# Kernel optimization log

Hardware: AMD Instinct MI355X
Metric: run time of the kernel (lower is better)

## Reference

```python
import jax, jax.numpy as jnp
import numpy as np

HIDDEN_DIM = 128


def setup_inputs() -> dict:
    key = jax.random.key(0)
    ks = jax.random.split(key, 7)
    n_edges, edge_dim, edge_hidden, d = 20000, 16, 128, HIDDEN_DIM
    h_v = jax.random.normal(ks[0], (n_edges, d), dtype=jnp.float32)
    h_w = jax.random.normal(ks[1], (n_edges, d), dtype=jnp.float32)
    edge_features = jax.random.normal(ks[2], (n_edges, edge_dim), dtype=jnp.float32)
    W1 = jax.random.normal(ks[3], (edge_dim, edge_hidden), dtype=jnp.float32) * (1.0 / np.sqrt(edge_dim))
    b1 = jnp.zeros((edge_hidden,), dtype=jnp.float32)
    W2 = jax.random.normal(ks[4], (edge_hidden, d * d), dtype=jnp.float32) * (1.0 / np.sqrt(edge_hidden))
    b2 = jnp.zeros((d * d,), dtype=jnp.float32)
    return {"h_v": h_v, "h_w": h_w, "edge_features": edge_features,
            "W1": W1, "b1": b1, "W2": W2, "b2": b2}


def reference(h_v, h_w, edge_features, W1, b1, W2, b2):
    d = HIDDEN_DIM
    # Edge MLP: edge_dim -> edge_hidden -> d*d
    hidden = jax.nn.relu(edge_features @ W1 + b1)          # (E, edge_hidden)
    A = (hidden @ W2 + b2).reshape(-1, d, d)               # (E, d, d) per-edge matrices
    # Batched matrix-vector product: messages_e = A_e @ h_w_e
    messages = jnp.einsum('eij,ej->ei', A, h_w)            # (E, d)
    return messages
```

## Files before the change

kernel.cpp:

```cpp
#include <hip/hip_runtime.h>

#define E_EDGES 20000
#define D_DIM   128
#define HS      136

#define NBA 136
#define NBH 313
#define NBC 320
#define NBD 250

#define SLAB_B 21504

typedef _Float16 f16x8 __attribute__((ext_vector_type(8)));
typedef _Float16 f16x2 __attribute__((ext_vector_type(2)));
typedef float    floatx4 __attribute__((ext_vector_type(4)));

union F8 { f16x8 v; f16x2 h2[4]; unsigned int u[4]; };

__device__ __forceinline__ unsigned short f32_to_f16(float f) {
    _Float16 h = (_Float16)f;
    return __builtin_bit_cast(unsigned short, h);
}

__device__ __forceinline__ void gload_lds16(const void* g, void* l) {
    __builtin_amdgcn_global_load_lds(
        (const __attribute__((address_space(1))) unsigned int*)g,
        (__attribute__((address_space(3))) unsigned int*)l, 16, 0, 0);
}

__global__ __launch_bounds__(256) void prep_all(
    const float* __restrict__ W2, const float* __restrict__ b2,
    const float* __restrict__ ef, const float* __restrict__ W1,
    const float* __restrict__ b1, const float* __restrict__ hw,
    uint4* __restrict__ bpf, char* __restrict__ hslab,
    unsigned short* __restrict__ hwb, float* __restrict__ outz)
{
    __shared__ __align__(16) char pmem[34816];
    const int bx = blockIdx.x;
    const int t  = threadIdx.x;

    if (bx < NBA) {
        const int h = bx;
        if (h < 129) {
            unsigned short* tile = (unsigned short*)pmem;
            const float* src = (h < 128) ? (W2 + (size_t)h * (D_DIM * D_DIM)) : b2;
            #pragma unroll
            for (int r = 0; r < 16; ++r) {
                const float4 v = ((const float4*)src)[r * 256 + t];
                int c   = (r * 256 + t) * 4;
                int col = c >> 7;
                int k   = c & 127;
                unsigned int u0 = f32_to_f16(v.x) | ((unsigned int)f32_to_f16(v.y) << 16);
                unsigned int u1 = f32_to_f16(v.z) | ((unsigned int)f32_to_f16(v.w) << 16);
                *(uint2*)&tile[col * 136 + k] = make_uint2(u0, u1);
            }
            __syncthreads();
            #pragma unroll
            for (int r2 = 0; r2 < 8; ++r2) {
                int cidx = r2 * 256 + t;
                int ll = cidx & 63;
                int nt = (cidx >> 6) & 3;
                int jq = (cidx >> 8) & 3;
                int ch = (cidx >> 10) & 1;
                int col = 64 * ch + 16 * nt + (ll & 15);
                int k0  = 32 * jq + 8 * (ll >> 4);
                bpf[(size_t)h * 2048 + cidx] = *(const uint4*)&tile[col * 136 + k0];
            }
        } else {
            #pragma unroll
            for (int r2 = 0; r2 < 8; ++r2)
                bpf[(size_t)h * 2048 + r2 * 256 + t] = make_uint4(0, 0, 0, 0);
        }
    } else if (bx < NBA + NBH) {
        float* W1s = (float*)pmem;
        float* b1s = (float*)(pmem + 8192);
        float (*efs)[17] = (float(*)[17])(pmem + 8704);
        const int b  = bx - NBA;
        const int e0 = b * 64;
        #pragma unroll
        for (int i = 0; i < 2; ++i)
            *(float4*)&W1s[(i * 256 + t) * 4] = ((const float4*)W1)[i * 256 + t];
        if (t < 32) *(float4*)&b1s[t * 4] = ((const float4*)b1)[t];
        {
            int e  = t >> 2;
            int k4 = (t & 3) * 4;
            int ge = e0 + e;
            float4 v = make_float4(0.f, 0.f, 0.f, 0.f);
            if (ge < E_EDGES) v = *(const float4*)(ef + (size_t)ge * 16 + k4);
            efs[e][k4 + 0] = v.x; efs[e][k4 + 1] = v.y;
            efs[e][k4 + 2] = v.z; efs[e][k4 + 3] = v.w;
        }
        __syncthreads();
        const int e  = t & 63;
        const int hg = t >> 6;
        const int ge = e0 + e;
        const bool valid = ge < E_EDGES;
        const int eg = ge / 80;
        const int re = ge - eg * 80;
        char* slab = hslab + (size_t)eg * SLAB_B + re * 264;
        float efr[16];
        #pragma unroll
        for (int k = 0; k < 16; ++k) efr[k] = efs[e][k];
        #pragma unroll 4
        for (int hi2 = 0; hi2 < 16; ++hi2) {
            const int h0 = hg * 32 + 2 * hi2;
            float2 bb = *(const float2*)&b1s[h0];
            float a0 = bb.x, a1 = bb.y;
            #pragma unroll
            for (int k = 0; k < 16; ++k) {
                float2 wv = *(const float2*)&W1s[k * 128 + h0];
                a0 += efr[k] * wv.x;
                a1 += efr[k] * wv.y;
            }
            unsigned int pk = (unsigned int)f32_to_f16(fmaxf(a0, 0.f))
                            | ((unsigned int)f32_to_f16(fmaxf(a1, 0.f)) << 16);
            if (valid) *(unsigned int*)(slab + h0 * 2) = pk;
        }
        if (hg == 0 && valid) {
            *(unsigned int*)(slab + 128 * 2) = 0x00003C00u;
            *(unsigned int*)(slab + 130 * 2) = 0u;
        }
    } else if (bx < NBA + NBH + NBC) {
        int i0 = (bx - NBA - NBH) * 256 + t;
        for (int i = i0; i < (E_EDGES * D_DIM) / 4; i += NBC * 256) {
            const float4 v = ((const float4*)hw)[i];
            union { unsigned short u16[4]; uint2 u2; } o;
            o.u16[0] = f32_to_f16(v.x);
            o.u16[1] = f32_to_f16(v.y);
            o.u16[2] = f32_to_f16(v.z);
            o.u16[3] = f32_to_f16(v.w);
            ((uint2*)hwb)[i] = o.u2;
        }
    } else {
        int i0 = (bx - NBA - NBH - NBC) * 256 + t;
        float4* o4 = (float4*)outz;
        for (int i = i0; i < (E_EDGES * D_DIM) / 4; i += NBD * 256)
            o4[i] = make_float4(0.f, 0.f, 0.f, 0.f);
    }
}

__global__ __launch_bounds__(256, 2)
void edge_main(const uint4* __restrict__ bpf, const char* __restrict__ hslab,
               const uint4* __restrict__ hwb, float* __restrict__ out) {
    __shared__ __align__(16) char slab[SLAB_B];
    const int bx  = blockIdx.x;
    const int ch  = (bx & 7) >> 2;
    const int eg  = (bx >> 3) * 4 + (bx & 3);
    if (eg >= 250) return;
    const int tid = threadIdx.x;
    const int jq  = tid >> 6;
    const int l   = tid & 63;
    const int l4  = l >> 4;
    const int lm  = l & 15;
    const int e0  = eg * 80;

    {
        const char* src = hslab + (size_t)eg * SLAB_B;
        for (int i = jq; i < 21; i += 4)
            gload_lds16(src + i * 1024 + l * 16, slab + i * 1024);
    }

    F8 hws[5];
    #pragma unroll
    for (int m = 0; m < 5; ++m)
        hws[m].v = ((const F8*)hwb)[(e0 + 16 * m + lm) * 16 + 4 * jq + l4].v;

    floatx4 C[5][4];
    #pragma unroll
    for (int m = 0; m < 5; ++m)
        #pragma unroll
        for (int nt = 0; nt < 4; ++nt)
            C[m][nt] = (floatx4){0.f, 0.f, 0.f, 0.f};

    __syncthreads();

    const f16x8* bpf8 = (const f16x8*)bpf;
    const int cbase = (ch * 4 + jq) * 256 + l;

    f16x8 B[2][4];
    auto loadB = [&](int h, f16x8 (&Bq)[4]) {
        const f16x8* p = bpf8 + (size_t)h * 2048 + cbase;
        #pragma unroll
        for (int nt = 0; nt < 4; ++nt)
            Bq[nt] = p[nt * 64];
    };
    auto loadHid = [&](int q, uint2 (&hid)[5]) {
        #pragma unroll
        for (int m = 0; m < 5; ++m)
            hid[m] = *(const uint2*)(slab + (16 * m + lm) * 264 + q * 8);
    };
    auto doH = [&](int h, const uint2 (&hid)[5]) {
        const int hh = h & 3, p = h & 1;
        #pragma unroll
        for (int m = 0; m < 5; ++m) {
            unsigned int s   = (hh < 2) ? hid[m].x : hid[m].y;
            unsigned int sel = (hh & 1) ? 0x03020302u : 0x01000100u;
            f16x2 d = __builtin_bit_cast(f16x2, __builtin_amdgcn_perm(0u, s, sel));
            F8 a;
            #pragma unroll
            for (int i = 0; i < 4; ++i) a.h2[i] = hws[m].h2[i] * d;
            #pragma unroll
            for (int nt = 0; nt < 4; ++nt)
                C[m][nt] = __builtin_amdgcn_mfma_f32_16x16x32_f16(a.v, B[p][nt], C[m][nt], 0, 0, 0);
        }
        loadB(h + 2, B[p]);
    };

    loadB(0, B[0]);
    loadB(1, B[1]);
    uint2 hidA[5], hidB[5];
    loadHid(0, hidA);
    for (int q = 0; q < 32; q += 2) {
        loadHid(q + 1, hidB);
        doH(4*q + 0, hidA); doH(4*q + 1, hidA); doH(4*q + 2, hidA); doH(4*q + 3, hidA);
        loadHid(q + 2, hidA);
        doH(4*q + 4, hidB); doH(4*q + 5, hidB); doH(4*q + 6, hidB); doH(4*q + 7, hidB);
    }
    doH(128, hidA); doH(129, hidA);
    doH(130, hidA); doH(131, hidA);

    #pragma unroll
    for (int m = 0; m < 5; ++m)
        #pragma unroll
        for (int nt = 0; nt < 4; ++nt)
            #pragma unroll
            for (int r = 0; r < 4; ++r)
                atomicAdd(&out[(size_t)(e0 + 16 * m + 4 * l4 + r) * D_DIM
                               + 64 * ch + 16 * nt + lm], C[m][nt][r]);
}

extern "C" void kernel_launch(void* const* d_in, const int* in_sizes, int n_in,
                              void* d_out, int out_size, void* d_ws, size_t ws_size,
                              hipStream_t stream) {
    const float* h_w = (const float*)d_in[1];
    const float* ef  = (const float*)d_in[2];
    const float* W1  = (const float*)d_in[3];
    const float* b1  = (const float*)d_in[4];
    const float* W2  = (const float*)d_in[5];
    const float* b2  = (const float*)d_in[6];
    float* out = (float*)d_out;

    char* ws = (char*)d_ws;
    uint4*          bpf   = (uint4*)ws;
    char*           hslab = ws + 4456448;
    unsigned short* hwb   = (unsigned short*)(ws + 4456448 + 5376000);

    hipLaunchKernelGGL(prep_all, dim3(NBA + NBH + NBC + NBD), dim3(256), 0, stream,
                       W2, b2, ef, W1, b1, h_w, bpf, hslab, hwb, out);
    hipLaunchKernelGGL(edge_main, dim3(504), dim3(256), 0, stream,
                       bpf, hslab, (const uint4*)hwb, out);
}
```

Baseline: 177.3 us.

## Split output columns four ways and reduce K-partials in LDS instead of atomics

Each block now covers 32 output columns instead of 64, with grid doubled to 1000 blocks and occupancy hint raised to 4 blocks per CU. The B-fragment layout in prep is reshuffled to match. The four waves' K-split partial sums are reduced through LDS, and wave 0 writes the result with plain stores. This removes the global float atomics and the separate zero-fill of the output. The trade-off is that each block re-reads the hidden slab and h_w, which roughly doubles L2 traffic for those, and the reduction adds several block barriers.

```diff
diff --git a/kernel.cpp b/kernel.cpp
--- a/kernel.cpp
+++ b/kernel.cpp
@@ -7,7 +7,6 @@
 #define NBA 136
 #define NBH 313
 #define NBC 320
-#define NBD 250
 
 #define SLAB_B 21504
 
@@ -33,7 +32,7 @@
     const float* __restrict__ ef, const float* __restrict__ W1,
     const float* __restrict__ b1, const float* __restrict__ hw,
     uint4* __restrict__ bpf, char* __restrict__ hslab,
-    unsigned short* __restrict__ hwb, float* __restrict__ outz)
+    unsigned short* __restrict__ hwb)
 {
     __shared__ __align__(16) char pmem[34816];
     const int bx = blockIdx.x;
@@ -59,10 +58,10 @@
             for (int r2 = 0; r2 < 8; ++r2) {
                 int cidx = r2 * 256 + t;
                 int ll = cidx & 63;
-                int nt = (cidx >> 6) & 3;
-                int jq = (cidx >> 8) & 3;
-                int ch = (cidx >> 10) & 1;
-                int col = 64 * ch + 16 * nt + (ll & 15);
+                int nt = (cidx >> 6) & 1;
+                int jq = (cidx >> 7) & 3;
+                int ch = (cidx >> 9) & 3;
+                int col = 32 * ch + 16 * nt + (ll & 15);
                 int k0  = 32 * jq + 8 * (ll >> 4);
                 bpf[(size_t)h * 2048 + cidx] = *(const uint4*)&tile[col * 136 + k0];
             }
@@ -120,7 +119,7 @@
             *(unsigned int*)(slab + 128 * 2) = 0x00003C00u;
             *(unsigned int*)(slab + 130 * 2) = 0u;
         }
-    } else if (bx < NBA + NBH + NBC) {
+    } else {
         int i0 = (bx - NBA - NBH) * 256 + t;
         for (int i = i0; i < (E_EDGES * D_DIM) / 4; i += NBC * 256) {
             const float4 v = ((const float4*)hw)[i];
@@ -131,22 +130,16 @@
             o.u16[3] = f32_to_f16(v.w);
             ((uint2*)hwb)[i] = o.u2;
         }
-    } else {
-        int i0 = (bx - NBA - NBH - NBC) * 256 + t;
-        float4* o4 = (float4*)outz;
-        for (int i = i0; i < (E_EDGES * D_DIM) / 4; i += NBD * 256)
-            o4[i] = make_float4(0.f, 0.f, 0.f, 0.f);
-    }
-}
-
-__global__ __launch_bounds__(256, 2)
+    }
+}
+
+__global__ __launch_bounds__(256, 4)
 void edge_main(const uint4* __restrict__ bpf, const char* __restrict__ hslab,
                const uint4* __restrict__ hwb, float* __restrict__ out) {
     __shared__ __align__(16) char slab[SLAB_B];
     const int bx  = blockIdx.x;
-    const int ch  = (bx & 7) >> 2;
-    const int eg  = (bx >> 3) * 4 + (bx & 3);
-    if (eg >= 250) return;
+    const int ch  = (bx & 7) >> 1;
+    const int eg  = (bx >> 3) * 2 + (bx & 1);
     const int tid = threadIdx.x;
     const int jq  = tid >> 6;
     const int l   = tid & 63;
@@ -165,29 +158,23 @@
     for (int m = 0; m < 5; ++m)
         hws[m].v = ((const F8*)hwb)[(e0 + 16 * m + lm) * 16 + 4 * jq + l4].v;
 
-    floatx4 C[5][4];
+    floatx4 C[5][2];
     #pragma unroll
     for (int m = 0; m < 5; ++m)
         #pragma unroll
-        for (int nt = 0; nt < 4; ++nt)
+        for (int nt = 0; nt < 2; ++nt)
             C[m][nt] = (floatx4){0.f, 0.f, 0.f, 0.f};
 
     __syncthreads();
 
     const f16x8* bpf8 = (const f16x8*)bpf;
-    const int cbase = (ch * 4 + jq) * 256 + l;
-
-    f16x8 B[2][4];
-    auto loadB = [&](int h, f16x8 (&Bq)[4]) {
+    const int cbase = ch * 512 + jq * 128 + l;
+
+    f16x8 B[2][2];
+    auto loadB = [&](int h, f16x8 (&Bq)[2]) {
         const f16x8* p = bpf8 + (size_t)h * 2048 + cbase;
-        #pragma unroll
-        for (int nt = 0; nt < 4; ++nt)
-            Bq[nt] = p[nt * 64];
-    };
-    auto loadHid = [&](int q, uint2 (&hid)[5]) {
-        #pragma unroll
-        for (int m = 0; m < 5; ++m)
-            hid[m] = *(const uint2*)(slab + (16 * m + lm) * 264 + q * 8);
+        Bq[0] = p[0];
+        Bq[1] = p[64];
     };
     auto doH = [&](int h, const uint2 (&hid)[5]) {
         const int hh = h & 3, p = h & 1;
@@ -199,34 +186,59 @@
             F8 a;
             #pragma unroll
             for (int i = 0; i < 4; ++i) a.h2[i] = hws[m].h2[i] * d;
-            #pragma unroll
-            for (int nt = 0; nt < 4; ++nt)
-                C[m][nt] = __builtin_amdgcn_mfma_f32_16x16x32_f16(a.v, B[p][nt], C[m][nt], 0, 0, 0);
+            C[m][0] = __builtin_amdgcn_mfma_f32_16x16x32_f16(a.v, B[p][0], C[m][0], 0, 0, 0);
+            C[m][1] = __builtin_amdgcn_mfma_f32_16x16x32_f16(a.v, B[p][1], C[m][1], 0, 0, 0);
         }
         loadB(h + 2, B[p]);
     };
 
     loadB(0, B[0]);
     loadB(1, B[1]);
-    uint2 hidA[5], hidB[5];
-    loadHid(0, hidA);
-    for (int q = 0; q < 32; q += 2) {
-        loadHid(q + 1, hidB);
-        doH(4*q + 0, hidA); doH(4*q + 1, hidA); doH(4*q + 2, hidA); doH(4*q + 3, hidA);
-        loadHid(q + 2, hidA);
-        doH(4*q + 4, hidB); doH(4*q + 5, hidB); doH(4*q + 6, hidB); doH(4*q + 7, hidB);
-    }
-    doH(128, hidA); doH(129, hidA);
-    doH(130, hidA); doH(131, hidA);
-
-    #pragma unroll
-    for (int m = 0; m < 5; ++m)
-        #pragma unroll
-        for (int nt = 0; nt < 4; ++nt)
-            #pragma unroll
-            for (int r = 0; r < 4; ++r)
-                atomicAdd(&out[(size_t)(e0 + 16 * m + 4 * l4 + r) * D_DIM
-                               + 64 * ch + 16 * nt + lm], C[m][nt][r]);
+    for (int q = 0; q < 33; ++q) {
+        uint2 hid[5];
+        #pragma unroll
+        for (int m = 0; m < 5; ++m)
+            hid[m] = *(const uint2*)(slab + (16 * m + lm) * 264 + q * 8);
+        doH(4 * q + 0, hid);
+        doH(4 * q + 1, hid);
+        doH(4 * q + 2, hid);
+        doH(4 * q + 3, hid);
+    }
+
+    float* red = (float*)slab;
+    #pragma unroll 1
+    for (int src = 1; src < 4; ++src) {
+        __syncthreads();
+        if (jq == src) {
+            #pragma unroll
+            for (int m = 0; m < 5; ++m)
+                #pragma unroll
+                for (int nt = 0; nt < 2; ++nt)
+                    #pragma unroll
+                    for (int r = 0; r < 4; ++r)
+                        red[((m * 2 + nt) * 4 + r) * 64 + l] = C[m][nt][r];
+        }
+        __syncthreads();
+        if (jq == 0) {
+            #pragma unroll
+            for (int m = 0; m < 5; ++m)
+                #pragma unroll
+                for (int nt = 0; nt < 2; ++nt)
+                    #pragma unroll
+                    for (int r = 0; r < 4; ++r)
+                        C[m][nt][r] += red[((m * 2 + nt) * 4 + r) * 64 + l];
+        }
+    }
+    if (jq == 0) {
+        #pragma unroll
+        for (int m = 0; m < 5; ++m)
+            #pragma unroll
+            for (int nt = 0; nt < 2; ++nt)
+                #pragma unroll
+                for (int r = 0; r < 4; ++r)
+                    out[(size_t)(e0 + 16 * m + 4 * l4 + r) * D_DIM
+                        + 32 * ch + 16 * nt + lm] = C[m][nt][r];
+    }
 }
 
 extern "C" void kernel_launch(void* const* d_in, const int* in_sizes, int n_in,
@@ -245,8 +257,8 @@
     char*           hslab = ws + 4456448;
     unsigned short* hwb   = (unsigned short*)(ws + 4456448 + 5376000);
 
-    hipLaunchKernelGGL(prep_all, dim3(NBA + NBH + NBC + NBD), dim3(256), 0, stream,
-                       W2, b2, ef, W1, b1, h_w, bpf, hslab, hwb, out);
-    hipLaunchKernelGGL(edge_main, dim3(504), dim3(256), 0, stream,
+    hipLaunchKernelGGL(prep_all, dim3(NBA + NBH + NBC), dim3(256), 0, stream,
+                       W2, b2, ef, W1, b1, h_w, bpf, hslab, hwb);
+    hipLaunchKernelGGL(edge_main, dim3(1000), dim3(256), 0, stream,
                        bpf, hslab, (const uint4*)hwb, out);
 }
```

Result: faster. 164.7 us (-7.1%).
